# Kernel optimization log

Measured on AMD Instinct MI355X. Metric: run time of the kernel, lower is better.

## Reference

```python
import jax, jax.numpy as jnp
import numpy as np

B, N, T, D = 16, 64, 128, 8
N_EMB, N_H = 64, 128
EPS = 1e-20


def _fully_connected_rel():
    # off-diagonal (receiver, sender) pairs of a fully connected graph
    off = np.ones((N, N)) - np.eye(N)
    rec_idx, send_idx = np.where(off)
    rel_rec = np.eye(N, dtype=np.float32)[rec_idx]
    rel_send = np.eye(N, dtype=np.float32)[send_idx]
    return jnp.asarray(rel_rec), jnp.asarray(rel_send)


def setup_inputs() -> dict:
    key = jax.random.key(0)
    ks = jax.random.split(key, 8)
    inputs = jax.random.normal(ks[0], (B, N, T, D), dtype=jnp.float32)
    rel_rec, rel_send = _fully_connected_rel()
    s = 0.05
    Wc = jax.random.normal(ks[1], (N_EMB, D), dtype=jnp.float32) * s
    bc = jnp.zeros((N_EMB,), jnp.float32)
    Ws = jax.random.normal(ks[2], (N_EMB, D), dtype=jnp.float32) * s
    bs = jnp.zeros((N_EMB,), jnp.float32)
    F_in = 2 * N_EMB
    W_ih = jax.random.normal(ks[3], (4 * N_H, F_in), dtype=jnp.float32) * s
    W_hh = jax.random.normal(ks[4], (4 * N_H, N_H), dtype=jnp.float32) * s
    b_ih = jnp.zeros((4 * N_H,), jnp.float32)
    b_hh = jnp.zeros((4 * N_H,), jnp.float32)
    return {"inputs": inputs, "rel_rec": rel_rec, "rel_send": rel_send,
            "Wc": Wc, "bc": bc, "Ws": Ws, "bs": bs,
            "W_ih": W_ih, "W_hh": W_hh, "b_ih": b_ih, "b_hh": b_hh}


def _gcn(x, rel_rec, rel_send, Wc, bc, Ws, bs):
    # x: [B, N, T, D]; rel_*: [E, N] one-hot
    senders = jnp.einsum('en,bntd->betd', rel_send, x)      # [B,E,T,D]
    receivers = jnp.einsum('en,bntd->betd', rel_rec, x)
    diff = receivers - senders
    spatial_norm = jnp.sqrt(jnp.sum(diff * diff, axis=-1))  # [B,E,T]
    vals = 1.0 / (spatial_norm + EPS)
    vals = jnp.transpose(vals, (0, 2, 1))                   # [B,T,E]
    # A = rel_send^T diag(vals) rel_rec, without the ExE diag_embed
    A = jnp.einsum('es,bte,er->btsr', rel_send, vals, rel_rec)  # [B,T,N,N]
    rowsum = jnp.sum(A, axis=-1, keepdims=True)
    A = A / jnp.clip(rowsum, 1e-12)                         # row-normalized
    x_t = jnp.transpose(x, (0, 2, 1, 3))                    # [B,T,N,D]
    x_conv = jnp.einsum('btnm,btmd->btnd', A, x_t) @ Wc.T + bc  # [B,T,N,emb]
    x_conv = jnp.transpose(x_conv, (0, 2, 1, 3))            # [B,N,T,emb]
    x_skip = x @ Ws.T + bs                                  # [B,N,T,emb]
    return jax.nn.selu(jnp.concatenate([x_skip, x_conv], axis=-1))


def _lstm(x_seq, W_ih, W_hh, b_ih, b_hh):
    # x_seq: [T, BN, F]
    BN = x_seq.shape[1]
    h0 = jnp.zeros((BN, N_H), x_seq.dtype)
    c0 = jnp.zeros((BN, N_H), x_seq.dtype)

    def step(carry, x_t):
        h, c = carry
        gates = x_t @ W_ih.T + b_ih + h @ W_hh.T + b_hh
        i, f, g, o = jnp.split(gates, 4, axis=-1)
        c = jax.nn.sigmoid(f) * c + jax.nn.sigmoid(i) * jnp.tanh(g)
        h = jax.nn.sigmoid(o) * jnp.tanh(c)
        return (h, c), None

    (h, c), _ = jax.lax.scan(step, (h0, c0), x_seq)
    return h


def reference(inputs, rel_rec, rel_send, Wc, bc, Ws, bs, W_ih, W_hh, b_ih, b_hh):
    b, n, t, _ = inputs.shape
    x = _gcn(inputs, rel_rec, rel_send, Wc, bc, Ws, bs)     # [B,N,T,2*emb]
    x_seq = jnp.transpose(x, (2, 0, 1, 3)).reshape(t, b * n, -1)
    h = _lstm(x_seq, W_ih, W_hh, b_ih, b_hh)                # [B*N, n_h]
    return h.reshape(b, n, -1)
```

## Files before the change

### kernel.cpp

```cpp
#include <hip/hip_runtime.h>
#include <hip/hip_bf16.h>


typedef _Float16 half8 __attribute__((ext_vector_type(8)));
typedef float f32x4 __attribute__((ext_vector_type(4)));

__device__ __forceinline__ float rcp_(float x){ return __builtin_amdgcn_rcpf(x); }
__device__ __forceinline__ float sigmoidf_(float x){ return rcp_(1.0f + __expf(-x)); }
__device__ __forceinline__ float tanhf_(float x){ return fmaf(-2.0f, rcp_(1.0f + __expf(2.0f*x)), 1.0f); }

__global__ __launch_bounds__(256) void prep_kernel(const float* __restrict__ W_ih,
                                                   const float* __restrict__ W_hh,
                                                   _Float16* __restrict__ wfrag){
  int gid = blockIdx.x*256 + threadIdx.x;
  int w    = gid >> 11;
  int i    = (gid >> 6) & 31;
  int lane = gid & 63;
  int src = i >> 4, kk = (i >> 2) & 3, cti = i & 3;
  int j = 16*w + 128*cti + (lane & 15);
  int kbase = 32*kk + 8*(lane >> 4);
  const float* W = src ? W_hh : W_ih;
  _Float16* dst = wfrag + (size_t)(((w*32 + i)*64 + lane) * 8);
  #pragma unroll
  for (int e = 0; e < 8; e++) dst[e] = (_Float16)W[j*128 + kbase + e];
}

__global__ __launch_bounds__(256) void gcn2_kernel(const float* __restrict__ x,
    const float* __restrict__ Wc, const float* __restrict__ bc,
    const float* __restrict__ Ws, const float* __restrict__ bs,
    _Float16* __restrict__ feat){
  __shared__ _Float16 W2[32*136];
  __shared__ _Float16 As16[4][64*72];
  __shared__ _Float16 zs16[4][64*40];

  int tid = threadIdx.x;
  int wav = tid >> 6, lane = tid & 63;
  int slice = blockIdx.x*4 + wav;
  int b = slice >> 7, t = slice & 127;
  int c = lane & 15, kq = lane >> 4;

  for (int idx = tid; idx < 32*136; idx += 256){
    int k = idx / 136, f = idx - k*136;
    float v = 0.f;
    if (f < 64){
      if (k < 8) v = Ws[f*8 + k];
      else if (k == 16) v = bs[f];
    } else if (f < 128){
      if (k >= 8 && k < 16) v = Wc[(f-64)*8 + (k-8)];
      else if (k == 16) v = bc[f-64];
    }
    W2[idx] = (_Float16)v;
  }

  _Float16* As_w = &As16[wav][0];
  _Float16* zs_w = &zs16[wav][0];

  const float* xrow = x + ((size_t)(b*64 + lane)*128 + t)*8;
  float4 xlo = *(const float4*)xrow;
  float4 xhi = *(const float4*)(xrow + 4);
  float xr[8] = {xlo.x, xlo.y, xlo.z, xlo.w, xhi.x, xhi.y, xhi.z, xhi.w};
  {
    half8 hx;
    #pragma unroll
    for (int d = 0; d < 8; d++) hx[d] = (_Float16)xr[d];
    half8 h1 = (half8){(_Float16)1.f,0,0,0,0,0,0,0};
    half8 h0 = (half8){0,0,0,0,0,0,0,0};
    *(half8*)(zs_w + lane*40)      = hx;
    *(half8*)(zs_w + lane*40 + 8)  = h1;
    *(half8*)(zs_w + lane*40 + 16) = h1;
    *(half8*)(zs_w + lane*40 + 24) = h0;
  }

  #pragma unroll 4
  for (int m = 0; m < 64; m++){
    float d2 = 0.f;
    #pragma unroll
    for (int d = 0; d < 8; d++){
      float xm = __int_as_float(__builtin_amdgcn_readlane(__float_as_int(xr[d]), m));
      float df = xm - xr[d];
      d2 = fmaf(df, df, d2);
    }
    float wv = (m == lane) ? 0.f : __frsqrt_rn(d2);
    As_w[m*72 + lane] = (_Float16)wv;
  }

  __syncthreads();

  half8 wfr[8];
  #pragma unroll
  for (int nt = 0; nt < 8; nt++){
    half8 tmp;
    #pragma unroll
    for (int e = 0; e < 8; e++) tmp[e] = W2[(8*kq + e)*136 + 16*nt + c];
    wfr[nt] = tmp;
  }

  half8 bx0, bx1;
  {
    half8 t0, t1;
    #pragma unroll
    for (int e = 0; e < 8; e++){
      t0[e] = zs_w[(8*kq + e)*40 + c];
      t1[e] = zs_w[(32 + 8*kq + e)*40 + c];
    }
    bx0 = t0; bx1 = t1;
  }

  const f32x4 zero4 = (f32x4){0.f,0.f,0.f,0.f};

  #pragma unroll
  for (int mt = 0; mt < 4; mt++){
    half8 aa0 = *(const half8*)(As_w + (16*mt + c)*72 + 8*kq);
    half8 aa1 = *(const half8*)(As_w + (16*mt + c)*72 + 32 + 8*kq);
    f32x4 cax = __builtin_amdgcn_mfma_f32_16x16x32_f16(aa0, bx0, zero4, 0,0,0);
    cax = __builtin_amdgcn_mfma_f32_16x16x32_f16(aa1, bx1, cax, 0,0,0);
    int bidx = ((lane & 48) | 8) << 2;
    #pragma unroll
    for (int e = 0; e < 4; e++){
      float rs = __int_as_float(__builtin_amdgcn_ds_bpermute(bidx, __float_as_int(cax[e])));
      float yv = cax[e] * rcp_(fmaxf(rs, 1e-12f));
      if (c < 8) zs_w[(16*mt + 4*kq + e)*40 + 8 + c] = (_Float16)yv;
    }
  }

  _Float16* st = As_w;
  int rr = lane >> 2, qq = lane & 3;
  #pragma unroll
  for (int mt = 0; mt < 4; mt++){
    half8 az = *(const half8*)(zs_w + (16*mt + c)*40 + 8*kq);
    #pragma unroll
    for (int nt = 0; nt < 8; nt++){
      f32x4 pc = __builtin_amdgcn_mfma_f32_16x16x32_f16(az, wfr[nt], zero4, 0,0,0);
      #pragma unroll
      for (int e = 0; e < 4; e++){
        float v = pc[e];
        v = (v > 0.f) ? 1.0507009873554805f*v
                      : 1.7580993408473766f*(__expf(v) - 1.0f);
        st[(4*kq + e)*132 + 16*nt + c] = (_Float16)v;
      }
    }
    asm volatile("s_waitcnt lgkmcnt(0)" ::: "memory");
    size_t obase = ((size_t)t*1024 + (size_t)b*64 + 16*mt + rr)*128 + qq*32;
    #pragma unroll
    for (int j = 0; j < 4; j++){
      half8 pk = *(const half8*)(st + rr*132 + qq*32 + 8*j);
      *(half8*)(feat + obase + 8*j) = pk;
    }
    asm volatile("s_waitcnt lgkmcnt(0)" ::: "memory");
  }
}

__global__ __launch_bounds__(512, 2) void lstm3_kernel(
    const _Float16* __restrict__ wfrag, const _Float16* __restrict__ feat,
    const float* __restrict__ b_ih, const float* __restrict__ b_hh,
    float* __restrict__ out){
  int tid = threadIdx.x;
  int w = tid >> 6, l = tid & 63;
  int blk = blockIdx.x;
  int r = l & 15, kq = l >> 4;
  __shared__ _Float16 h_lds[2][544];

  half8 bf[32];
  const _Float16* wb = wfrag + (size_t)w*(32*64*8);
  #pragma unroll
  for (int i = 0; i < 32; i++)
    bf[i] = *(const half8*)(wb + (size_t)(i*64 + l)*8);

  f32x4 biasx4[4];
  #pragma unroll
  for (int cti = 0; cti < 4; cti++){
    int j = 16*w + 128*cti + r;
    float bv = b_ih[j] + b_hh[j];
    biasx4[cti] = (f32x4){bv, bv, bv, bv};
  }

  for (int idx = tid; idx < 544; idx += 512) h_lds[0][idx] = (_Float16)0.f;

  float cc = 0.f;
  const f32x4 zero4 = (f32x4){0.f,0.f,0.f,0.f};

  const size_t arow_s = (size_t)(blk*4 + (r >> 2));
  const int atl = r & 3;
  const int habase = (r & 3)*134 + 8*kq;
  const int hwoff = kq*134 + 16*w + r;

  half8 afA[4], afB[4];
  f32x4 accxA[4], accxB[4];

#define LOADAF(AF, G) {                                                       \
    int gg = (G) > 31 ? 31 : (G);                                             \
    const _Float16* fb = feat + ((size_t)(4*gg + atl)*1024 + arow_s)*128 + 8*kq; \
    AF[0] = *(const half8*)(fb);                                              \
    AF[1] = *(const half8*)(fb + 32);                                         \
    AF[2] = *(const half8*)(fb + 64);                                         \
    AF[3] = *(const half8*)(fb + 96);                                         \
  }

  LOADAF(afA, 0)
  #pragma unroll
  for (int cti = 0; cti < 4; cti++)
    accxA[cti] = __builtin_amdgcn_mfma_f32_16x16x32_f16(afA[0], bf[cti], biasx4[cti], 0,0,0);
  #pragma unroll
  for (int kk = 1; kk < 4; kk++)
    #pragma unroll
    for (int cti = 0; cti < 4; cti++)
      accxA[cti] = __builtin_amdgcn_mfma_f32_16x16x32_f16(afA[kk], bf[kk*4+cti], accxA[cti], 0,0,0);
  LOADAF(afB, 1)
  LOADAF(afA, 2)
  __syncthreads();

#define SEL(A) ((kq & 2) ? ((kq & 1) ? A[3] : A[2]) : ((kq & 1) ? A[1] : A[0]))

#define STEP3(TL, ACCU, ACCB, AFB_, GN)                                       \
  {                                                                           \
    half8 ha[4];                                                              \
    _Pragma("unroll")                                                         \
    for (int kk = 0; kk < 4; kk++)                                            \
      ha[kk] = *(const half8*)(&h_lds[(TL)&1][habase + 32*kk]);               \
    _Pragma("unroll")                                                         \
    for (int cti = 0; cti < 4; cti++){                                        \
      if ((TL) == 0)                                                          \
        ACCB[cti] = __builtin_amdgcn_mfma_f32_16x16x32_f16(AFB_[0], bf[cti], biasx4[cti], 0,0,0); \
      else                                                                    \
        ACCB[cti] = __builtin_amdgcn_mfma_f32_16x16x32_f16(AFB_[(TL)], bf[(TL)*4+cti], ACCB[cti], 0,0,0); \
    }                                                                         \
    if ((TL) == 3) LOADAF(AFB_, GN)                                           \
    f32x4 acc0, acc1, acc2, acc3;                                             \
    acc0 = __builtin_amdgcn_mfma_f32_16x16x32_f16(ha[0], bf[16], zero4, 0,0,0); \
    acc1 = __builtin_amdgcn_mfma_f32_16x16x32_f16(ha[0], bf[17], zero4, 0,0,0); \
    acc2 = __builtin_amdgcn_mfma_f32_16x16x32_f16(ha[0], bf[18], zero4, 0,0,0); \
    acc3 = __builtin_amdgcn_mfma_f32_16x16x32_f16(ha[0], bf[19], zero4, 0,0,0); \
    _Pragma("unroll")                                                         \
    for (int kk = 1; kk < 4; kk++){                                           \
      acc0 = __builtin_amdgcn_mfma_f32_16x16x32_f16(ha[kk], bf[16+kk*4+0], acc0, 0,0,0); \
      acc1 = __builtin_amdgcn_mfma_f32_16x16x32_f16(ha[kk], bf[16+kk*4+1], acc1, 0,0,0); \
      acc2 = __builtin_amdgcn_mfma_f32_16x16x32_f16(ha[kk], bf[16+kk*4+2], acc2, 0,0,0); \
      acc3 = __builtin_amdgcn_mfma_f32_16x16x32_f16(ha[kk], bf[16+kk*4+3], acc3, 0,0,0); \
    }                                                                         \
    float g0_ = SEL(acc0) + ACCU[0][(TL)];                                    \
    float g1_ = SEL(acc1) + ACCU[1][(TL)];                                    \
    float g2_ = SEL(acc2) + ACCU[2][(TL)];                                    \
    float g3_ = SEL(acc3) + ACCU[3][(TL)];                                    \
    float c_ = fmaf(sigmoidf_(g1_), cc, sigmoidf_(g0_)*tanhf_(g2_));          \
    cc = c_;                                                                  \
    float h_ = sigmoidf_(g3_)*tanhf_(c_);                                     \
    h_lds[1-((TL)&1)][hwoff] = (_Float16)h_;                                  \
    asm volatile("s_waitcnt lgkmcnt(0)" ::: "memory");                        \
    __builtin_amdgcn_s_barrier();                                             \
  }

  for (int i = 0; i < 16; ++i){
    STEP3(0, accxA, accxB, afB, 0)
    STEP3(1, accxA, accxB, afB, 0)
    STEP3(2, accxA, accxB, afB, 0)
    STEP3(3, accxA, accxB, afB, 2*i+3)
    STEP3(0, accxB, accxA, afA, 0)
    STEP3(1, accxB, accxA, afA, 0)
    STEP3(2, accxB, accxA, afA, 0)
    STEP3(3, accxB, accxA, afA, 2*i+4)
  }
#undef STEP3
#undef SEL
#undef LOADAF

  out[((size_t)blk*4 + kq)*128 + 16*w + r] = (float)h_lds[0][hwoff];
}

extern "C" void kernel_launch(void* const* d_in, const int* in_sizes, int n_in,
                              void* d_out, int out_size, void* d_ws, size_t ws_size,
                              hipStream_t stream) {
  const float* x    = (const float*)d_in[0];
  const float* Wc   = (const float*)d_in[3];
  const float* bc   = (const float*)d_in[4];
  const float* Ws   = (const float*)d_in[5];
  const float* bs   = (const float*)d_in[6];
  const float* W_ih = (const float*)d_in[7];
  const float* W_hh = (const float*)d_in[8];
  const float* b_ih = (const float*)d_in[9];
  const float* b_hh = (const float*)d_in[10];
  float* out = (float*)d_out;

  _Float16* wfrag = (_Float16*)d_ws;
  _Float16* feat  = (_Float16*)((char*)d_ws + 262144);

  prep_kernel<<<64, 256, 0, stream>>>(W_ih, W_hh, wfrag);
  gcn2_kernel<<<512, 256, 0, stream>>>(x, Wc, bc, Ws, bs, feat);
  lstm3_kernel<<<256, 512, 0, stream>>>(wfrag, feat, b_ih, b_hh, out);
}
```

Baseline: 118.4 us.

## Hoist LSTM input projection into separate GEMM kernel and shrink recurrent blocks

Moves the input-to-gate projection (x@W_ih^T + biases) out of the sequential LSTM loop into a new parallel GEMM kernel that writes fp16 gate pre-activations for all timesteps to a workspace buffer. The recurrent kernel now handles 2 sequences per 256-thread block (512 blocks) instead of 4 per 512-thread block, and in each step does only the h@W_hh MFMAs plus a prefetched half4 load of the precomputed gates. This takes the input MFMAs off the serial critical path and spreads the recurrence over more blocks. In exchange it writes and reads a large fp16 intermediate (T*B*N*512) through global memory, adds a kernel launch, and stores the input projection at fp16 precision.

```diff
diff --git a/kernel.cpp b/kernel.cpp
--- a/kernel.cpp
+++ b/kernel.cpp
@@ -3,6 +3,7 @@
 
 
 typedef _Float16 half8 __attribute__((ext_vector_type(8)));
+typedef _Float16 half4 __attribute__((ext_vector_type(4)));
 typedef float f32x4 __attribute__((ext_vector_type(4)));
 
 __device__ __forceinline__ float rcp_(float x){ return __builtin_amdgcn_rcpf(x); }
@@ -150,120 +151,144 @@
   }
 }
 
-__global__ __launch_bounds__(512, 2) void lstm3_kernel(
+__global__ __launch_bounds__(256) void xgemm2_kernel(
     const _Float16* __restrict__ wfrag, const _Float16* __restrict__ feat,
     const float* __restrict__ b_ih, const float* __restrict__ b_hh,
+    _Float16* __restrict__ gx){
+  int blk = blockIdx.x;
+  int t = blk >> 4, gq = blk & 15;
+  int tid = threadIdx.x;
+  int v = tid >> 6, l = tid & 63;
+  int c = l & 15, kq = l >> 4;
+
+  __shared__ _Float16 fs[64*136];
+  __shared__ _Float16 gxo[16*512];
+
+  #pragma unroll
+  for (int i = 0; i < 4; i++){
+    int flat = tid + 256*i;
+    int n = flat >> 4, c8 = flat & 15;
+    half8 vd = *(const half8*)(feat + ((size_t)t*1024 + 64*gq + n)*128 + c8*8);
+    *(half8*)(fs + n*136 + c8*8) = vd;
+  }
+
+  half8 bfr[8][4];
+  float bb[8];
+  #pragma unroll
+  for (int ct = 0; ct < 8; ct++){
+    #pragma unroll
+    for (int kk = 0; kk < 4; kk++)
+      bfr[ct][kk] = *(const half8*)(wfrag + (size_t)((ct*32 + kk*4 + v)*64 + l)*8);
+    int j = 128*v + 16*ct + c;
+    bb[ct] = b_ih[j] + b_hh[j];
+  }
+  __syncthreads();
+
+  for (int m = 0; m < 4; m++){
+    half8 af[4];
+    #pragma unroll
+    for (int kk = 0; kk < 4; kk++)
+      af[kk] = *(const half8*)(fs + (16*m + c)*136 + 32*kk + 8*kq);
+    #pragma unroll
+    for (int ct = 0; ct < 8; ct++){
+      f32x4 acc = (f32x4){bb[ct], bb[ct], bb[ct], bb[ct]};
+      #pragma unroll
+      for (int kk = 0; kk < 4; kk++)
+        acc = __builtin_amdgcn_mfma_f32_16x16x32_f16(af[kk], bfr[ct][kk], acc, 0, 0, 0);
+      #pragma unroll
+      for (int e = 0; e < 4; e++)
+        gxo[(4*kq + e)*512 + (16*ct + c)*4 + v] = (_Float16)acc[e];
+    }
+    __syncthreads();
+    size_t obase = ((size_t)t*1024 + 64*gq + 16*m)*512;
+    #pragma unroll
+    for (int j = 0; j < 4; j++){
+      half8 pk = *(const half8*)(gxo + tid*32 + j*8);
+      *(half8*)(gx + obase + tid*32 + j*8) = pk;
+    }
+    __syncthreads();
+  }
+}
+
+__global__ __launch_bounds__(256, 2) void lstm4_kernel(
+    const _Float16* __restrict__ wfrag, const _Float16* __restrict__ gx,
     float* __restrict__ out){
   int tid = threadIdx.x;
   int w = tid >> 6, l = tid & 63;
   int blk = blockIdx.x;
   int r = l & 15, kq = l >> 4;
-  __shared__ _Float16 h_lds[2][544];
+  __shared__ _Float16 h_lds[2][2*136];
 
   half8 bf[32];
-  const _Float16* wb = wfrag + (size_t)w*(32*64*8);
-  #pragma unroll
-  for (int i = 0; i < 32; i++)
-    bf[i] = *(const half8*)(wb + (size_t)(i*64 + l)*8);
-
-  f32x4 biasx4[4];
-  #pragma unroll
-  for (int cti = 0; cti < 4; cti++){
-    int j = 16*w + 128*cti + r;
-    float bv = b_ih[j] + b_hh[j];
-    biasx4[cti] = (f32x4){bv, bv, bv, bv};
-  }
-
-  for (int idx = tid; idx < 544; idx += 512) h_lds[0][idx] = (_Float16)0.f;
+  #pragma unroll
+  for (int m = 0; m < 8; m++){
+    int ct = w + 4*m;
+    int w8 = ct & 7, cti = ct >> 3;
+    #pragma unroll
+    for (int kk = 0; kk < 4; kk++)
+      bf[m*4 + kk] = *(const half8*)(wfrag + (size_t)((w8*32 + 16 + kk*4 + cti)*64 + l)*8);
+  }
+
+  for (int idx = tid; idx < 2*136; idx += 256){
+    h_lds[0][idx] = (_Float16)0.f; h_lds[1][idx] = (_Float16)0.f;
+  }
 
   float cc = 0.f;
   const f32x4 zero4 = (f32x4){0.f,0.f,0.f,0.f};
 
-  const size_t arow_s = (size_t)(blk*4 + (r >> 2));
-  const int atl = r & 3;
-  const int habase = (r & 3)*134 + 8*kq;
-  const int hwoff = kq*134 + 16*w + r;
-
-  half8 afA[4], afB[4];
-  f32x4 accxA[4], accxB[4];
-
-#define LOADAF(AF, G) {                                                       \
-    int gg = (G) > 31 ? 31 : (G);                                             \
-    const _Float16* fb = feat + ((size_t)(4*gg + atl)*1024 + arow_s)*128 + 8*kq; \
-    AF[0] = *(const half8*)(fb);                                              \
-    AF[1] = *(const half8*)(fb + 32);                                         \
-    AF[2] = *(const half8*)(fb + 64);                                         \
-    AF[3] = *(const half8*)(fb + 96);                                         \
-  }
-
-  LOADAF(afA, 0)
-  #pragma unroll
-  for (int cti = 0; cti < 4; cti++)
-    accxA[cti] = __builtin_amdgcn_mfma_f32_16x16x32_f16(afA[0], bf[cti], biasx4[cti], 0,0,0);
-  #pragma unroll
-  for (int kk = 1; kk < 4; kk++)
-    #pragma unroll
-    for (int cti = 0; cti < 4; cti++)
-      accxA[cti] = __builtin_amdgcn_mfma_f32_16x16x32_f16(afA[kk], bf[kk*4+cti], accxA[cti], 0,0,0);
-  LOADAF(afB, 1)
-  LOADAF(afA, 2)
+  const int samp = kq & 1, uu = kq >> 1;
+  const int hh = uu*64 + 16*w + r;
+  const size_t gxbase = ((size_t)(blk*2 + samp)*128 + hh)*4;
+  const int haoff = (r & 1)*136 + 8*kq;
+  const int hwoff = samp*136 + hh;
+
+  half4 ga = *(const half4*)(gx + gxbase);
+  half4 gb = *(const half4*)(gx + 524288 + gxbase);
   __syncthreads();
 
-#define SEL(A) ((kq & 2) ? ((kq & 1) ? A[3] : A[2]) : ((kq & 1) ? A[1] : A[0]))
-
-#define STEP3(TL, ACCU, ACCB, AFB_, GN)                                       \
+#define STEP4(T, GU, TL, PR, PW)                                              \
   {                                                                           \
+    half4 gcur = GU;                                                          \
+    GU = *(const half4*)(gx + (size_t)(TL)*524288 + gxbase);                  \
     half8 ha[4];                                                              \
     _Pragma("unroll")                                                         \
     for (int kk = 0; kk < 4; kk++)                                            \
-      ha[kk] = *(const half8*)(&h_lds[(TL)&1][habase + 32*kk]);               \
+      ha[kk] = *(const half8*)(&h_lds[PR][haoff + 32*kk]);                    \
+    f32x4 acc[8];                                                             \
     _Pragma("unroll")                                                         \
-    for (int cti = 0; cti < 4; cti++){                                        \
-      if ((TL) == 0)                                                          \
-        ACCB[cti] = __builtin_amdgcn_mfma_f32_16x16x32_f16(AFB_[0], bf[cti], biasx4[cti], 0,0,0); \
-      else                                                                    \
-        ACCB[cti] = __builtin_amdgcn_mfma_f32_16x16x32_f16(AFB_[(TL)], bf[(TL)*4+cti], ACCB[cti], 0,0,0); \
-    }                                                                         \
-    if ((TL) == 3) LOADAF(AFB_, GN)                                           \
-    f32x4 acc0, acc1, acc2, acc3;                                             \
-    acc0 = __builtin_amdgcn_mfma_f32_16x16x32_f16(ha[0], bf[16], zero4, 0,0,0); \
-    acc1 = __builtin_amdgcn_mfma_f32_16x16x32_f16(ha[0], bf[17], zero4, 0,0,0); \
-    acc2 = __builtin_amdgcn_mfma_f32_16x16x32_f16(ha[0], bf[18], zero4, 0,0,0); \
-    acc3 = __builtin_amdgcn_mfma_f32_16x16x32_f16(ha[0], bf[19], zero4, 0,0,0); \
+    for (int m = 0; m < 8; m++)                                               \
+      acc[m] = __builtin_amdgcn_mfma_f32_16x16x32_f16(ha[0], bf[m*4], zero4, 0,0,0); \
     _Pragma("unroll")                                                         \
     for (int kk = 1; kk < 4; kk++){                                           \
-      acc0 = __builtin_amdgcn_mfma_f32_16x16x32_f16(ha[kk], bf[16+kk*4+0], acc0, 0,0,0); \
-      acc1 = __builtin_amdgcn_mfma_f32_16x16x32_f16(ha[kk], bf[16+kk*4+1], acc1, 0,0,0); \
-      acc2 = __builtin_amdgcn_mfma_f32_16x16x32_f16(ha[kk], bf[16+kk*4+2], acc2, 0,0,0); \
-      acc3 = __builtin_amdgcn_mfma_f32_16x16x32_f16(ha[kk], bf[16+kk*4+3], acc3, 0,0,0); \
+      _Pragma("unroll")                                                       \
+      for (int m = 0; m < 8; m++)                                             \
+        acc[m] = __builtin_amdgcn_mfma_f32_16x16x32_f16(ha[kk], bf[m*4 + kk], acc[m], 0,0,0); \
     }                                                                         \
-    float g0_ = SEL(acc0) + ACCU[0][(TL)];                                    \
-    float g1_ = SEL(acc1) + ACCU[1][(TL)];                                    \
-    float g2_ = SEL(acc2) + ACCU[2][(TL)];                                    \
-    float g3_ = SEL(acc3) + ACCU[3][(TL)];                                    \
-    float c_ = fmaf(sigmoidf_(g1_), cc, sigmoidf_(g0_)*tanhf_(g2_));          \
+    float gv[4];                                                              \
+    _Pragma("unroll")                                                         \
+    for (int g = 0; g < 4; g++){                                              \
+      float vA = samp ? acc[2*g][1]   : acc[2*g][0];                          \
+      float vB = samp ? acc[2*g+1][1] : acc[2*g+1][0];                        \
+      gv[g] = (uu ? vB : vA) + (float)gcur[g];                                \
+    }                                                                         \
+    float c_ = fmaf(sigmoidf_(gv[1]), cc, sigmoidf_(gv[0])*tanhf_(gv[2]));    \
     cc = c_;                                                                  \
-    float h_ = sigmoidf_(g3_)*tanhf_(c_);                                     \
-    h_lds[1-((TL)&1)][hwoff] = (_Float16)h_;                                  \
+    float h_ = sigmoidf_(gv[3])*tanhf_(c_);                                   \
+    h_lds[PW][hwoff] = (_Float16)h_;                                          \
     asm volatile("s_waitcnt lgkmcnt(0)" ::: "memory");                        \
     __builtin_amdgcn_s_barrier();                                             \
   }
 
-  for (int i = 0; i < 16; ++i){
-    STEP3(0, accxA, accxB, afB, 0)
-    STEP3(1, accxA, accxB, afB, 0)
-    STEP3(2, accxA, accxB, afB, 0)
-    STEP3(3, accxA, accxB, afB, 2*i+3)
-    STEP3(0, accxB, accxA, afA, 0)
-    STEP3(1, accxB, accxA, afA, 0)
-    STEP3(2, accxB, accxA, afA, 0)
-    STEP3(3, accxB, accxA, afA, 2*i+4)
-  }
-#undef STEP3
-#undef SEL
-#undef LOADAF
-
-  out[((size_t)blk*4 + kq)*128 + 16*w + r] = (float)h_lds[0][hwoff];
+  for (int it = 0; it < 64; ++it){
+    int t0 = 2*it, t1 = 2*it + 1;
+    int l0 = (t0 + 2 > 127) ? 127 : t0 + 2;
+    int l1 = (t1 + 2 > 127) ? 127 : t1 + 2;
+    STEP4(t0, ga, l0, 0, 1)
+    STEP4(t1, gb, l1, 1, 0)
+  }
+#undef STEP4
+
+  out[((size_t)(blk*2 + samp))*128 + hh] = (float)h_lds[0][hwoff];
 }
 
 extern "C" void kernel_launch(void* const* d_in, const int* in_sizes, int n_in,
@@ -282,8 +307,10 @@
 
   _Float16* wfrag = (_Float16*)d_ws;
   _Float16* feat  = (_Float16*)((char*)d_ws + 262144);
+  _Float16* gxbuf = (_Float16*)((char*)d_ws + 33816576);
 
   prep_kernel<<<64, 256, 0, stream>>>(W_ih, W_hh, wfrag);
   gcn2_kernel<<<512, 256, 0, stream>>>(x, Wc, bc, Ws, bs, feat);
-  lstm3_kernel<<<256, 512, 0, stream>>>(wfrag, feat, b_ih, b_hh, out);
-}
+  xgemm2_kernel<<<2048, 256, 0, stream>>>(wfrag, feat, b_ih, b_hh, gxbuf);
+  lstm4_kernel<<<512, 256, 0, stream>>>(wfrag, gxbuf, out);
+}
```

Result: slower. 169.6 us (+43.3%).

## Interleave two independent LSTM row groups per block to hide recurrence latency

Applied to the files above, without the earlier changes.

The LSTM kernel now processes two independent groups of 4 rows per block, halving the grid to 128 blocks, and interleaves their timesteps. While one group's recurrent h@W_hh MFMAs run, the other group's gate nonlinearities and h write are done, so the dependent chain of MFMA, activation and barrier for one group overlaps with work from the other. Input-projection MFMAs are spread one k-slice per segment, and feature loads are issued one fragment at a time. This trades fewer resident blocks (fewer CUs busy) for better latency hiding inside each block, plus a tail step computed outside the loop for the second group.

```diff
diff --git a/kernel.cpp b/kernel.cpp
--- a/kernel.cpp
+++ b/kernel.cpp
@@ -150,7 +150,7 @@
   }
 }
 
-__global__ __launch_bounds__(512, 2) void lstm3_kernel(
+__global__ __launch_bounds__(512, 2) void lstm5_kernel(
     const _Float16* __restrict__ wfrag, const _Float16* __restrict__ feat,
     const float* __restrict__ b_ih, const float* __restrict__ b_hh,
     float* __restrict__ out){
@@ -158,7 +158,7 @@
   int w = tid >> 6, l = tid & 63;
   int blk = blockIdx.x;
   int r = l & 15, kq = l >> 4;
-  __shared__ _Float16 h_lds[2][544];
+  __shared__ _Float16 h_lds[2][2][544];
 
   half8 bf[32];
   const _Float16* wb = wfrag + (size_t)w*(32*64*8);
@@ -166,104 +166,125 @@
   for (int i = 0; i < 32; i++)
     bf[i] = *(const half8*)(wb + (size_t)(i*64 + l)*8);
 
-  f32x4 biasx4[4];
+  float bias[4];
   #pragma unroll
   for (int cti = 0; cti < 4; cti++){
     int j = 16*w + 128*cti + r;
-    float bv = b_ih[j] + b_hh[j];
-    biasx4[cti] = (f32x4){bv, bv, bv, bv};
-  }
-
-  for (int idx = tid; idx < 544; idx += 512) h_lds[0][idx] = (_Float16)0.f;
-
-  float cc = 0.f;
+    bias[cti] = b_ih[j] + b_hh[j];
+  }
+
+  for (int idx = tid; idx < 544; idx += 512){
+    h_lds[0][0][idx] = (_Float16)0.f;
+    h_lds[1][0][idx] = (_Float16)0.f;
+  }
+
+  float ccA = 0.f, ccB = 0.f;
   const f32x4 zero4 = (f32x4){0.f,0.f,0.f,0.f};
 
-  const size_t arow_s = (size_t)(blk*4 + (r >> 2));
   const int atl = r & 3;
+  const size_t arowA = (size_t)(blk*8 + (r >> 2));
+  const size_t arowB = arowA + 4;
   const int habase = (r & 3)*134 + 8*kq;
-  const int hwoff = kq*134 + 16*w + r;
-
-  half8 afA[4], afB[4];
-  f32x4 accxA[4], accxB[4];
-
-#define LOADAF(AF, G) {                                                       \
-    int gg = (G) > 31 ? 31 : (G);                                             \
-    const _Float16* fb = feat + ((size_t)(4*gg + atl)*1024 + arow_s)*128 + 8*kq; \
-    AF[0] = *(const half8*)(fb);                                              \
-    AF[1] = *(const half8*)(fb + 32);                                         \
-    AF[2] = *(const half8*)(fb + 64);                                         \
-    AF[3] = *(const half8*)(fb + 96);                                         \
-  }
-
-  LOADAF(afA, 0)
-  #pragma unroll
-  for (int cti = 0; cti < 4; cti++)
-    accxA[cti] = __builtin_amdgcn_mfma_f32_16x16x32_f16(afA[0], bf[cti], biasx4[cti], 0,0,0);
-  #pragma unroll
-  for (int kk = 1; kk < 4; kk++)
-    #pragma unroll
-    for (int cti = 0; cti < 4; cti++)
-      accxA[cti] = __builtin_amdgcn_mfma_f32_16x16x32_f16(afA[kk], bf[kk*4+cti], accxA[cti], 0,0,0);
-  LOADAF(afB, 1)
-  LOADAF(afA, 2)
+  const int hwoff  = kq*134 + 16*w + r;
+
+  f32x4 xA0[4], xA1[4], xB0[4], xB1[4];
+  f32x4 haccA[4], haccB[4];
+  half8 afA0, afA1, afB0, afB1;
+
+#define FADDR(AR, WL, KK) \
+  (feat + (((size_t)(4*(WL) + atl))*1024 + (AR))*128 + 8*kq + 32*(KK))
+
+  #pragma unroll
+  for (int kk = 0; kk < 4; kk++){
+    half8 fa = *(const half8*)FADDR(arowA, 0, kk);
+    half8 fb = *(const half8*)FADDR(arowB, 0, kk);
+    #pragma unroll
+    for (int cti = 0; cti < 4; cti++){
+      f32x4 cia = (kk == 0) ? (f32x4){bias[cti],bias[cti],bias[cti],bias[cti]} : xA0[cti];
+      f32x4 cib = (kk == 0) ? (f32x4){bias[cti],bias[cti],bias[cti],bias[cti]} : xB0[cti];
+      xA0[cti] = __builtin_amdgcn_mfma_f32_16x16x32_f16(fa, bf[kk*4+cti], cia, 0,0,0);
+      xB0[cti] = __builtin_amdgcn_mfma_f32_16x16x32_f16(fb, bf[kk*4+cti], cib, 0,0,0);
+    }
+  }
+  afA0 = *(const half8*)FADDR(arowA, 1, 0);
+  afB0 = *(const half8*)FADDR(arowB, 1, 0);
+  #pragma unroll
+  for (int cti = 0; cti < 4; cti++){ haccB[cti] = zero4; xB1[cti] = zero4; }
   __syncthreads();
 
 #define SEL(A) ((kq & 2) ? ((kq & 1) ? A[3] : A[2]) : ((kq & 1) ? A[1] : A[0]))
 
-#define STEP3(TL, ACCU, ACCB, AFB_, GN)                                       \
-  {                                                                           \
-    half8 ha[4];                                                              \
-    _Pragma("unroll")                                                         \
-    for (int kk = 0; kk < 4; kk++)                                            \
-      ha[kk] = *(const half8*)(&h_lds[(TL)&1][habase + 32*kk]);               \
-    _Pragma("unroll")                                                         \
-    for (int cti = 0; cti < 4; cti++){                                        \
-      if ((TL) == 0)                                                          \
-        ACCB[cti] = __builtin_amdgcn_mfma_f32_16x16x32_f16(AFB_[0], bf[cti], biasx4[cti], 0,0,0); \
-      else                                                                    \
-        ACCB[cti] = __builtin_amdgcn_mfma_f32_16x16x32_f16(AFB_[(TL)], bf[(TL)*4+cti], ACCB[cti], 0,0,0); \
-    }                                                                         \
-    if ((TL) == 3) LOADAF(AFB_, GN)                                           \
-    f32x4 acc0, acc1, acc2, acc3;                                             \
-    acc0 = __builtin_amdgcn_mfma_f32_16x16x32_f16(ha[0], bf[16], zero4, 0,0,0); \
-    acc1 = __builtin_amdgcn_mfma_f32_16x16x32_f16(ha[0], bf[17], zero4, 0,0,0); \
-    acc2 = __builtin_amdgcn_mfma_f32_16x16x32_f16(ha[0], bf[18], zero4, 0,0,0); \
-    acc3 = __builtin_amdgcn_mfma_f32_16x16x32_f16(ha[0], bf[19], zero4, 0,0,0); \
-    _Pragma("unroll")                                                         \
-    for (int kk = 1; kk < 4; kk++){                                           \
-      acc0 = __builtin_amdgcn_mfma_f32_16x16x32_f16(ha[kk], bf[16+kk*4+0], acc0, 0,0,0); \
-      acc1 = __builtin_amdgcn_mfma_f32_16x16x32_f16(ha[kk], bf[16+kk*4+1], acc1, 0,0,0); \
-      acc2 = __builtin_amdgcn_mfma_f32_16x16x32_f16(ha[kk], bf[16+kk*4+2], acc2, 0,0,0); \
-      acc3 = __builtin_amdgcn_mfma_f32_16x16x32_f16(ha[kk], bf[16+kk*4+3], acc3, 0,0,0); \
-    }                                                                         \
-    float g0_ = SEL(acc0) + ACCU[0][(TL)];                                    \
-    float g1_ = SEL(acc1) + ACCU[1][(TL)];                                    \
-    float g2_ = SEL(acc2) + ACCU[2][(TL)];                                    \
-    float g3_ = SEL(acc3) + ACCU[3][(TL)];                                    \
-    float c_ = fmaf(sigmoidf_(g1_), cc, sigmoidf_(g0_)*tanhf_(g2_));          \
-    cc = c_;                                                                  \
-    float h_ = sigmoidf_(g3_)*tanhf_(c_);                                     \
-    h_lds[1-((TL)&1)][hwoff] = (_Float16)h_;                                  \
-    asm volatile("s_waitcnt lgkmcnt(0)" ::: "memory");                        \
-    __builtin_amdgcn_s_barrier();                                             \
-  }
-
-  for (int i = 0; i < 16; ++i){
-    STEP3(0, accxA, accxB, afB, 0)
-    STEP3(1, accxA, accxB, afB, 0)
-    STEP3(2, accxA, accxB, afB, 0)
-    STEP3(3, accxA, accxB, afB, 2*i+3)
-    STEP3(0, accxB, accxA, afA, 0)
-    STEP3(1, accxB, accxA, afA, 0)
-    STEP3(2, accxB, accxA, afA, 0)
-    STEP3(3, accxB, accxA, afA, 2*i+4)
-  }
-#undef STEP3
+#define SEG(GIDX, TL, HACCG, XN, AFU, AFL, AROW, WLD, KKL,                     \
+            OGIDX, OTL, HACCO, XCO, CCO)                                       \
+  {                                                                            \
+    AFL = *(const half8*)FADDR(AROW, WLD, KKL);                                \
+    half8 ha0 = *(const half8*)(&h_lds[GIDX][(TL)&1][habase]);                 \
+    half8 ha1 = *(const half8*)(&h_lds[GIDX][(TL)&1][habase + 32]);            \
+    half8 ha2 = *(const half8*)(&h_lds[GIDX][(TL)&1][habase + 64]);            \
+    half8 ha3 = *(const half8*)(&h_lds[GIDX][(TL)&1][habase + 96]);            \
+    _Pragma("unroll")                                                          \
+    for (int cti = 0; cti < 4; cti++){                                         \
+      f32x4 a = __builtin_amdgcn_mfma_f32_16x16x32_f16(ha0, bf[16+cti], zero4, 0,0,0); \
+      a = __builtin_amdgcn_mfma_f32_16x16x32_f16(ha1, bf[20+cti], a, 0,0,0);   \
+      a = __builtin_amdgcn_mfma_f32_16x16x32_f16(ha2, bf[24+cti], a, 0,0,0);   \
+      a = __builtin_amdgcn_mfma_f32_16x16x32_f16(ha3, bf[28+cti], a, 0,0,0);   \
+      HACCG[cti] = a;                                                          \
+    }                                                                          \
+    _Pragma("unroll")                                                          \
+    for (int cti = 0; cti < 4; cti++){                                         \
+      f32x4 ci = ((TL) == 0) ? (f32x4){bias[cti],bias[cti],bias[cti],bias[cti]} \
+                             : XN[cti];                                        \
+      XN[cti] = __builtin_amdgcn_mfma_f32_16x16x32_f16(AFU, bf[(TL)*4+cti], ci, 0,0,0); \
+    }                                                                          \
+    float g0_ = SEL(HACCO[0]) + XCO[0][(OTL)];                                 \
+    float g1_ = SEL(HACCO[1]) + XCO[1][(OTL)];                                 \
+    float g2_ = SEL(HACCO[2]) + XCO[2][(OTL)];                                 \
+    float g3_ = SEL(HACCO[3]) + XCO[3][(OTL)];                                 \
+    float c_ = fmaf(sigmoidf_(g1_), CCO, sigmoidf_(g0_)*tanhf_(g2_));          \
+    CCO = c_;                                                                  \
+    float h_ = sigmoidf_(g3_)*tanhf_(c_);                                      \
+    h_lds[OGIDX][1-((OTL)&1)][hwoff] = (_Float16)h_;                           \
+    asm volatile("s_waitcnt lgkmcnt(0)" ::: "memory");                         \
+    __builtin_amdgcn_s_barrier();                                              \
+  }
+
+  for (int it = 0; it < 16; ++it){
+    int wa  = 2*it + 1;
+    int wbp = (2*it + 2 > 31) ? 31 : 2*it + 2;
+    int wc  = (2*it + 3 > 31) ? 31 : 2*it + 3;
+    SEG(0,0, haccA, xA1, afA0, afA1, arowA, wa,  1,  1, 3, haccB, xB1, ccB)
+    SEG(1,0, haccB, xB1, afB0, afB1, arowB, wa,  1,  0, 0, haccA, xA0, ccA)
+    SEG(0,1, haccA, xA1, afA1, afA0, arowA, wa,  2,  1, 0, haccB, xB0, ccB)
+    SEG(1,1, haccB, xB1, afB1, afB0, arowB, wa,  2,  0, 1, haccA, xA0, ccA)
+    SEG(0,2, haccA, xA1, afA0, afA1, arowA, wa,  3,  1, 1, haccB, xB0, ccB)
+    SEG(1,2, haccB, xB1, afB0, afB1, arowB, wa,  3,  0, 2, haccA, xA0, ccA)
+    SEG(0,3, haccA, xA1, afA1, afA0, arowA, wbp, 0,  1, 2, haccB, xB0, ccB)
+    SEG(1,3, haccB, xB1, afB1, afB0, arowB, wbp, 0,  0, 3, haccA, xA0, ccA)
+    SEG(0,0, haccA, xA0, afA0, afA1, arowA, wbp, 1,  1, 3, haccB, xB0, ccB)
+    SEG(1,0, haccB, xB0, afB0, afB1, arowB, wbp, 1,  0, 0, haccA, xA1, ccA)
+    SEG(0,1, haccA, xA0, afA1, afA0, arowA, wbp, 2,  1, 0, haccB, xB1, ccB)
+    SEG(1,1, haccB, xB0, afB1, afB0, arowB, wbp, 2,  0, 1, haccA, xA1, ccA)
+    SEG(0,2, haccA, xA0, afA0, afA1, arowA, wbp, 3,  1, 1, haccB, xB1, ccB)
+    SEG(1,2, haccB, xB0, afB0, afB1, arowB, wbp, 3,  0, 2, haccA, xA1, ccA)
+    SEG(0,3, haccA, xA0, afA1, afA0, arowA, wc,  0,  1, 2, haccB, xB1, ccB)
+    SEG(1,3, haccB, xB0, afB1, afB0, arowB, wc,  0,  0, 3, haccA, xA1, ccA)
+  }
+#undef SEG
+
+  float outB;
+  {
+    float g0_ = SEL(haccB[0]) + xB1[0][3];
+    float g1_ = SEL(haccB[1]) + xB1[1][3];
+    float g2_ = SEL(haccB[2]) + xB1[2][3];
+    float g3_ = SEL(haccB[3]) + xB1[3][3];
+    float c_ = fmaf(sigmoidf_(g1_), ccB, sigmoidf_(g0_)*tanhf_(g2_));
+    outB = sigmoidf_(g3_)*tanhf_(c_);
+  }
 #undef SEL
-#undef LOADAF
-
-  out[((size_t)blk*4 + kq)*128 + 16*w + r] = (float)h_lds[0][hwoff];
+#undef FADDR
+
+  out[((size_t)(blk*8 + kq))*128 + 16*w + r]     = (float)h_lds[0][0][hwoff];
+  out[((size_t)(blk*8 + 4 + kq))*128 + 16*w + r] = outB;
 }
 
 extern "C" void kernel_launch(void* const* d_in, const int* in_sizes, int n_in,
@@ -285,5 +306,5 @@
 
   prep_kernel<<<64, 256, 0, stream>>>(W_ih, W_hh, wfrag);
   gcn2_kernel<<<512, 256, 0, stream>>>(x, Wc, bc, Ws, bs, feat);
-  lstm3_kernel<<<256, 512, 0, stream>>>(wfrag, feat, b_ih, b_hh, out);
+  lstm5_kernel<<<128, 512, 0, stream>>>(wfrag, feat, b_ih, b_hh, out);
 }
```

New measurement: 280.0 us. 2.37x slower.
